# Kernel tuning notes

Hardware: AMD Instinct MI355X
Metric: run time of the kernel (lower is better)

Reference implementation:

```python
import jax, jax.numpy as jnp
import numpy as np

XS, YS = 512, 512  # xsize+1, ysize+1 with init args 511, 511


def _grid_sample_align_corners(img, gx, gy):
    """Bilinear grid_sample with align_corners=True, zeros padding.
    img: [C, H, W]; gx, gy: [X, Y] normalized coords in grid_sample convention
    (gx indexes W, gy indexes H). Returns [C, X, Y]."""
    C, H, W = img.shape
    x = (gx + 1.0) * 0.5 * (W - 1)
    y = (gy + 1.0) * 0.5 * (H - 1)
    x0 = jnp.floor(x)
    y0 = jnp.floor(y)
    wx1 = x - x0
    wy1 = y - y0
    out = jnp.zeros((C,) + gx.shape, img.dtype)
    for dy in (0, 1):
        for dx in (0, 1):
            xi = x0 + dx
            yi = y0 + dy
            w = (wx1 if dx else 1.0 - wx1) * (wy1 if dy else 1.0 - wy1)
            valid = (xi >= 0) & (xi <= W - 1) & (yi >= 0) & (yi <= H - 1)
            xc = jnp.clip(xi, 0, W - 1).astype(jnp.int32)
            yc = jnp.clip(yi, 0, H - 1).astype(jnp.int32)
            v = img[:, yc, xc]  # [C, X, Y]
            out = out + v * (w * valid.astype(img.dtype))[None]
    return out


def _per_batch(a, b, c, pnts, coors, contain):
    # a/b/c: [C,H,W] feature maps; pnts: [P,2] in [0,1]; coors: [P,3] int; contain: [P] int
    keep = contain > 0
    # route invalid pillars to an out-of-bounds index -> dropped by scatter
    cx = jnp.where(keep, coors[:, 1], XS)
    cy = jnp.where(keep, coors[:, 2], YS)
    grid = jnp.full((XS, YS, 2), -2.0, a.dtype)
    grid = grid.at[cx, cy, :].set(pnts * 2.0 - 1.0, mode='drop')
    mask = jnp.zeros((XS, YS), a.dtype).at[cx, cy].set(1.0, mode='drop')
    gx, gy = grid[..., 0], grid[..., 1]
    fa = _grid_sample_align_corners(a, gx, gy) * mask[None]
    fb = _grid_sample_align_corners(b, gx, gy) * mask[None]
    fc = _grid_sample_align_corners(c, gx, gy) * mask[None]
    return fa, fb, fc


def reference(c3, c4, c5, dynamic_img, pillar_img_pts, rgb_coors, contains_rgb):
    fa, fb, fc = jax.vmap(_per_batch)(c3, c4, c5, pillar_img_pts, rgb_coors, contains_rgb)
    # weighted fusion of the three scales, weights broadcast over channel dim
    return (fa * dynamic_img[:, 0:1]
            + fb * dynamic_img[:, 1:2]
            + fc * dynamic_img[:, 2:3])


def setup_inputs() -> dict:
    key = jax.random.key(0)
    ks = jax.random.split(key, 7)
    B, C, P = 4, 64, 20000
    c3 = jax.random.normal(ks[0], (B, C, 48, 160), jnp.float32)
    c4 = jax.random.normal(ks[1], (B, C, 24, 80), jnp.float32)
    c5 = jax.random.normal(ks[2], (B, C, 12, 40), jnp.float32)
    dynamic_img = jax.random.uniform(ks[3], (B, 3, XS, YS), jnp.float32)
    pillar_img_pts = jax.random.uniform(ks[4], (B, P, 2), jnp.float32)
    rgb_coors = jax.random.randint(ks[5], (B, P, 3), 0, 512, jnp.int32)
    contains_rgb = jax.random.randint(ks[6], (B, P), 0, 2, jnp.int32)
    return {"c3": c3, "c4": c4, "c5": c5, "dynamic_img": dynamic_img,
            "pillar_img_pts": pillar_img_pts, "rgb_coors": rgb_coors,
            "contains_rgb": contains_rgb}
```

## Files before the change

### kernel.cpp

```cpp
#include <hip/hip_runtime.h>
#include <cstddef>

#define XSZ 512
#define YSZ 512
#define NB  4
#define NC  64
#define NP  20000
#define H3 48
#define W3 160
#define H4 24
#define W4 80
#define H5 12
#define W5 40
#define HW3 (H3*W3)
#define HW4 (H4*W4)
#define HW5 (H5*W5)
#define SLOT_CAP 64

#define FILL_BLOCKS 256
#define T3_TILES (NB * ((HW3 + 63) / 64))
#define T4_TILES (NB * ((HW4 + 63) / 64))
#define T5_TILES (NB * ((HW5 + 63) / 64))

typedef float f4 __attribute__((ext_vector_type(4)));

__global__ void __launch_bounds__(256)
k_init(int4* __restrict__ winner4,
       const float* __restrict__ c3, const float* __restrict__ c4,
       const float* __restrict__ c5,
       float* __restrict__ c3t, float* __restrict__ c4t, float* __restrict__ c5t) {
    int blk = blockIdx.x;
    if (blk < FILL_BLOCKS) {
        int base = blk * 1024 + threadIdx.x;
        int4 m1 = make_int4(-1, -1, -1, -1);
        winner4[base      ] = m1;
        winner4[base + 256] = m1;
        winner4[base + 512] = m1;
        winner4[base + 768] = m1;
        return;
    }
    __shared__ float lds[NC * 65];
    int t = blk - FILL_BLOCKS;
    const float* in; float* outp; int HW, tpb;
    if (t < T3_TILES)                      { in = c3; outp = c3t; HW = HW3; tpb = 120; }
    else if ((t -= T3_TILES) < T4_TILES)   { in = c4; outp = c4t; HW = HW4; tpb = 30; }
    else { t -= T4_TILES;                    in = c5; outp = c5t; HW = HW5; tpb = 8; }
    int b  = t / tpb;
    int p0 = (t - b * tpb) * 64;
    int lane = threadIdx.x & 63, wave = threadIdx.x >> 6;
    const float* in_b  = in   + (size_t)b * NC * HW;
    float*       out_b = outp + (size_t)b * HW * NC;

    int p = p0 + lane;
    if (p < HW) {
        for (int ch = wave; ch < NC; ch += 4)
            lds[ch * 65 + lane] = in_b[(size_t)ch * HW + p];
    }
    __syncthreads();
    for (int pp = wave; pp < 64; pp += 4) {
        int pq = p0 + pp;
        if (pq < HW) out_b[(size_t)pq * NC + lane] = lds[lane * 65 + pp];
    }
}

__global__ void __launch_bounds__(256)
k_scatter(const int* __restrict__ coors, const int* __restrict__ contains,
          int* __restrict__ winner) {
    int idx = blockIdx.x * blockDim.x + threadIdx.x;
    if (idx >= NB * NP) return;
    if (contains[idx] <= 0) return;
    int b  = idx / NP;
    int p  = idx - b * NP;
    int cx = coors[idx * 3 + 1];
    int cy = coors[idx * 3 + 2];
    if ((unsigned)cx >= XSZ || (unsigned)cy >= YSZ) return;
    atomicMax(&winner[((size_t)b * XSZ + cx) * YSZ + cy], p);
}

__device__ __forceinline__ float bilinT(const float* __restrict__ img, int H, int W,
                                        float px, float py, int c) {
    float gx = px * 2.0f - 1.0f;
    float gy = py * 2.0f - 1.0f;
    float x = (gx + 1.0f) * 0.5f * (float)(W - 1);
    float y = (gy + 1.0f) * 0.5f * (float)(H - 1);
    float x0f = floorf(x), y0f = floorf(y);
    float wx1 = x - x0f,   wy1 = y - y0f;
    float wx0 = 1.0f - wx1, wy0 = 1.0f - wy1;
    int x0 = (int)x0f, y0 = (int)y0f;
    float acc = 0.0f;
#pragma unroll
    for (int dy = 0; dy < 2; ++dy) {
#pragma unroll
        for (int dx = 0; dx < 2; ++dx) {
            int xi = x0 + dx, yi = y0 + dy;
            bool valid = (xi >= 0) && (xi <= W - 1) && (yi >= 0) && (yi <= H - 1);
            int xc = min(max(xi, 0), W - 1);
            int yc = min(max(yi, 0), H - 1);
            float w = (dx ? wx1 : wx0) * (dy ? wy1 : wy0);
            float v = img[(size_t)(yc * W + xc) * NC + c];
            acc = fmaf(v, valid ? w : 0.0f, acc);
        }
    }
    return acc;
}

__device__ __forceinline__ float bilinG(const float* __restrict__ img, int H, int W,
                                        float px, float py, int c, int sChan) {
    float gx = px * 2.0f - 1.0f;
    float gy = py * 2.0f - 1.0f;
    float x = (gx + 1.0f) * 0.5f * (float)(W - 1);
    float y = (gy + 1.0f) * 0.5f * (float)(H - 1);
    float x0f = floorf(x), y0f = floorf(y);
    float wx1 = x - x0f,   wy1 = y - y0f;
    float wx0 = 1.0f - wx1, wy0 = 1.0f - wy1;
    int x0 = (int)x0f, y0 = (int)y0f;
    float acc = 0.0f;
#pragma unroll
    for (int dy = 0; dy < 2; ++dy) {
#pragma unroll
        for (int dx = 0; dx < 2; ++dx) {
            int xi = x0 + dx, yi = y0 + dy;
            bool valid = (xi >= 0) && (xi <= W - 1) && (yi >= 0) && (yi <= H - 1);
            int xc = min(max(xi, 0), W - 1);
            int yc = min(max(yi, 0), H - 1);
            float w = (dx ? wx1 : wx0) * (dy ? wy1 : wy0);
            float v = img[(size_t)(yc * W + xc) + (size_t)c * sChan];
            acc = fmaf(v, valid ? w : 0.0f, acc);
        }
    }
    return acc;
}

__global__ void __launch_bounds__(256)
k_fused(const float* __restrict__ pnts, const int* __restrict__ winner,
        const float* __restrict__ i3t, const float* __restrict__ i4t,
        const float* __restrict__ i5t, const float* __restrict__ dyn,
        float* __restrict__ out) {
    __shared__ float vec[SLOT_CAP * 65];
    __shared__ unsigned short smap[YSZ];
    __shared__ unsigned short slist[YSZ];
    __shared__ unsigned short ylist[YSZ];
    __shared__ int cnt;

    int bx = blockIdx.x;
    int b = bx >> 9, x = bx & 511;
    int tid = threadIdx.x;
    if (tid == 0) cnt = 0;
    __syncthreads();

    const int2* wrow2 = (const int2*)(winner + ((size_t)b * XSZ + x) * YSZ);
    int2 r2 = wrow2[tid];
    {
        int y0 = tid * 2;
        int pv0 = r2.x, pv1 = r2.y;
        int s0 = 0xFFFF, s1 = 0xFFFF;
        if (pv0 >= 0) { s0 = atomicAdd(&cnt, 1); slist[s0] = (unsigned short)pv0;
                        ylist[s0] = (unsigned short)y0; }
        if (pv1 >= 0) { s1 = atomicAdd(&cnt, 1); slist[s1] = (unsigned short)pv1;
                        ylist[s1] = (unsigned short)(y0 + 1); }
        smap[y0]     = (unsigned short)s0;
        smap[y0 + 1] = (unsigned short)s1;
    }
    __syncthreads();
    int n = cnt;
    int nB = min(n, SLOT_CAP);

    int wave = tid >> 6, lane = tid & 63;
    const float* i3b = i3t + (size_t)b * HW3 * NC;
    const float* i4b = i4t + (size_t)b * HW4 * NC;
    const float* i5b = i5t + (size_t)b * HW5 * NC;
    for (int s = wave; s < nB; s += 4) {
        int p = slist[s], y = ylist[s];
        int idx = b * NP + p;
        float px = pnts[idx * 2], py = pnts[idx * 2 + 1];
        float fa = bilinT(i3b, H3, W3, px, py, lane);
        float fb = bilinT(i4b, H4, W4, px, py, lane);
        float fc = bilinT(i5b, H5, W5, px, py, lane);
        size_t dbase = (((size_t)b * 3) * XSZ + x) * YSZ + y;
        float d0 = dyn[dbase];
        float d1 = dyn[dbase + (size_t)XSZ * YSZ];
        float d2 = dyn[dbase + (size_t)2 * XSZ * YSZ];
        vec[s * 65 + lane] = fa * d0 + fb * d1 + fc * d2;
    }
    __syncthreads();

    int lane_c = tid >> 7;
    int t7 = tid & 127;
    int y4 = t7 << 2;
    int s0 = smap[y4], s1 = smap[y4 + 1], s2 = smap[y4 + 2], s3 = smap[y4 + 3];
    bool h0 = s0 < SLOT_CAP, h1 = s1 < SLOT_CAP;
    bool h2 = s2 < SLOT_CAP, h3 = s3 < SLOT_CAP;
    size_t obase = (size_t)b * NC * XSZ * YSZ + (size_t)x * YSZ + y4;
    for (int cb = 0; cb < NC; cb += 2) {
        int c = cb + lane_c;
        f4 v = (f4)(0.0f);
        if (h0) v.x = vec[s0 * 65 + c];
        if (h1) v.y = vec[s1 * 65 + c];
        if (h2) v.z = vec[s2 * 65 + c];
        if (h3) v.w = vec[s3 * 65 + c];
        *(f4*)(out + obase + (size_t)c * (XSZ * YSZ)) = v;
    }

    if (n > SLOT_CAP) {
        __syncthreads();
        for (int s = SLOT_CAP + wave; s < n; s += 4) {
            int p = slist[s], y = ylist[s];
            int idx = b * NP + p;
            float px = pnts[idx * 2], py = pnts[idx * 2 + 1];
            float fa = bilinT(i3b, H3, W3, px, py, lane);
            float fb = bilinT(i4b, H4, W4, px, py, lane);
            float fc = bilinT(i5b, H5, W5, px, py, lane);
            size_t dbase = (((size_t)b * 3) * XSZ + x) * YSZ + y;
            float d0 = dyn[dbase];
            float d1 = dyn[dbase + (size_t)XSZ * YSZ];
            float d2 = dyn[dbase + (size_t)2 * XSZ * YSZ];
            out[(((size_t)b * NC + lane) * XSZ + x) * YSZ + y] =
                fa * d0 + fb * d1 + fc * d2;
        }
    }
}

__global__ void __launch_bounds__(256)
k_samp_fb(const int* __restrict__ coors, const int* __restrict__ contains,
          const float* __restrict__ pnts, const int* __restrict__ winner,
          const float* __restrict__ i3, const float* __restrict__ i4,
          const float* __restrict__ i5, const float* __restrict__ dyn,
          float* __restrict__ out) {
    int nw   = gridDim.x << 2;
    int wv   = (blockIdx.x << 2) + (threadIdx.x >> 6);
    int lane = threadIdx.x & 63;
    for (int idx = wv; idx < NB * NP; idx += nw) {
        if (contains[idx] <= 0) continue;
        int b = idx / NP;
        int p = idx - b * NP;
        int cx = coors[idx * 3 + 1];
        int cy = coors[idx * 3 + 2];
        if ((unsigned)cx >= XSZ || (unsigned)cy >= YSZ) continue;
        if (winner[((size_t)b * XSZ + cx) * YSZ + cy] != p) continue;
        float px = pnts[idx * 2], py = pnts[idx * 2 + 1];
        float fa = bilinG(i3 + (size_t)b * NC * HW3, H3, W3, px, py, lane, HW3);
        float fb = bilinG(i4 + (size_t)b * NC * HW4, H4, W4, px, py, lane, HW4);
        float fc = bilinG(i5 + (size_t)b * NC * HW5, H5, W5, px, py, lane, HW5);
        size_t dbase = (((size_t)b * 3) * XSZ + cx) * YSZ + cy;
        float d0 = dyn[dbase];
        float d1 = dyn[dbase + (size_t)XSZ * YSZ];
        float d2 = dyn[dbase + (size_t)2 * XSZ * YSZ];
        out[(((size_t)b * NC + lane) * XSZ + cx) * YSZ + cy] = fa * d0 + fb * d1 + fc * d2;
    }
}

__global__ void k_zero4(float4* __restrict__ p, long n4) {
    long i = (long)blockIdx.x * blockDim.x + threadIdx.x;
    long stride = (long)gridDim.x * blockDim.x;
    for (; i < n4; i += stride) p[i] = make_float4(0.f, 0.f, 0.f, 0.f);
}

extern "C" void kernel_launch(void* const* d_in, const int* in_sizes, int n_in,
                              void* d_out, int out_size, void* d_ws, size_t ws_size,
                              hipStream_t stream) {
    const float* c3       = (const float*)d_in[0];
    const float* c4       = (const float*)d_in[1];
    const float* c5       = (const float*)d_in[2];
    const float* dyn      = (const float*)d_in[3];
    const float* pnts     = (const float*)d_in[4];
    const int*   coors    = (const int*)d_in[5];
    const int*   contains = (const int*)d_in[6];
    float* out = (float*)d_out;

    char* ws = (char*)d_ws;
    size_t off = 0;
    int* winner = (int*)(ws + off);   off += (size_t)NB * XSZ * YSZ * 4;
    float* c3t  = (float*)(ws + off); off += (size_t)NB * NC * HW3 * 4;
    float* c4t  = (float*)(ws + off); off += (size_t)NB * NC * HW4 * 4;
    float* c5t  = (float*)(ws + off); off += (size_t)NB * NC * HW5 * 4;
    size_t t_need = off;
    bool useT = (ws_size >= t_need);

    int npts = NB * NP;
    int init_blocks = useT ? (FILL_BLOCKS + T3_TILES + T4_TILES + T5_TILES)
                           : FILL_BLOCKS;
    k_init<<<init_blocks, 256, 0, stream>>>((int4*)winner, c3, c4, c5,
                                            c3t, c4t, c5t);
    k_scatter<<<(npts + 255) / 256, 256, 0, stream>>>(coors, contains, winner);

    if (useT) {
        k_fused<<<NB * XSZ, 256, 0, stream>>>(pnts, winner, c3t, c4t, c5t,
                                              dyn, out);
    } else {
        long n4 = (long)out_size / 4;
        k_zero4<<<8192, 256, 0, stream>>>((float4*)out, n4);
        k_samp_fb<<<2048, 256, 0, stream>>>(coors, contains, pnts, winner,
                                            c3, c4, c5, dyn, out);
    }
}
```

Baseline: 78.55 us.

## Merge init, scatter and gather into one cooperative persistent kernel

Replaces the three separate launches (winner fill plus transpose, scatter, fused gather) with one cooperative kernel of 1024 blocks. Grid-wide syncs separate the phases, and each block then handles two x-rows with 4 pixels per thread and a larger slot cap. The goal is to remove launch gaps and kernel-boundary drains. In exchange it relies on cooperative launch co-residency, adds the cost of grid syncs, and falls back to a memset-based path if the launch fails.

```diff
diff --git a/kernel.cpp b/kernel.cpp
--- a/kernel.cpp
+++ b/kernel.cpp
@@ -1,4 +1,5 @@
 #include <hip/hip_runtime.h>
+#include <hip/hip_cooperative_groups.h>
 #include <cstddef>
 
 #define XSZ 512
@@ -15,51 +16,205 @@
 #define HW3 (H3*W3)
 #define HW4 (H4*W4)
 #define HW5 (H5*W5)
-#define SLOT_CAP 64
-
-#define FILL_BLOCKS 256
+#define HWO (XSZ*YSZ)
+
+#define GRID2 1024
+#define CAP   96
+
 #define T3_TILES (NB * ((HW3 + 63) / 64))
 #define T4_TILES (NB * ((HW4 + 63) / 64))
 #define T5_TILES (NB * ((HW5 + 63) / 64))
+#define T_TOTAL  (T3_TILES + T4_TILES + T5_TILES)
+#define SCAT_BLOCKS ((NB * NP + 255) / 256)
 
 typedef float f4 __attribute__((ext_vector_type(4)));
 
-__global__ void __launch_bounds__(256)
-k_init(int4* __restrict__ winner4,
-       const float* __restrict__ c3, const float* __restrict__ c4,
-       const float* __restrict__ c5,
-       float* __restrict__ c3t, float* __restrict__ c4t, float* __restrict__ c5t) {
-    int blk = blockIdx.x;
-    if (blk < FILL_BLOCKS) {
-        int base = blk * 1024 + threadIdx.x;
-        int4 m1 = make_int4(-1, -1, -1, -1);
-        winner4[base      ] = m1;
-        winner4[base + 256] = m1;
-        winner4[base + 512] = m1;
-        winner4[base + 768] = m1;
-        return;
-    }
-    __shared__ float lds[NC * 65];
-    int t = blk - FILL_BLOCKS;
-    const float* in; float* outp; int HW, tpb;
-    if (t < T3_TILES)                      { in = c3; outp = c3t; HW = HW3; tpb = 120; }
-    else if ((t -= T3_TILES) < T4_TILES)   { in = c4; outp = c4t; HW = HW4; tpb = 30; }
-    else { t -= T4_TILES;                    in = c5; outp = c5t; HW = HW5; tpb = 8; }
-    int b  = t / tpb;
-    int p0 = (t - b * tpb) * 64;
-    int lane = threadIdx.x & 63, wave = threadIdx.x >> 6;
-    const float* in_b  = in   + (size_t)b * NC * HW;
-    float*       out_b = outp + (size_t)b * HW * NC;
-
-    int p = p0 + lane;
-    if (p < HW) {
-        for (int ch = wave; ch < NC; ch += 4)
-            lds[ch * 65 + lane] = in_b[(size_t)ch * HW + p];
-    }
+__device__ __forceinline__ float bilinT(const float* __restrict__ img, int H, int W,
+                                        float px, float py, int c) {
+    float gx = px * 2.0f - 1.0f;
+    float gy = py * 2.0f - 1.0f;
+    float x = (gx + 1.0f) * 0.5f * (float)(W - 1);
+    float y = (gy + 1.0f) * 0.5f * (float)(H - 1);
+    float x0f = floorf(x), y0f = floorf(y);
+    float wx1 = x - x0f,   wy1 = y - y0f;
+    float wx0 = 1.0f - wx1, wy0 = 1.0f - wy1;
+    int x0 = (int)x0f, y0 = (int)y0f;
+    float acc = 0.0f;
+#pragma unroll
+    for (int dy = 0; dy < 2; ++dy) {
+#pragma unroll
+        for (int dx = 0; dx < 2; ++dx) {
+            int xi = x0 + dx, yi = y0 + dy;
+            bool valid = (xi >= 0) && (xi <= W - 1) && (yi >= 0) && (yi <= H - 1);
+            int xc = min(max(xi, 0), W - 1);
+            int yc = min(max(yi, 0), H - 1);
+            float w = (dx ? wx1 : wx0) * (dy ? wy1 : wy0);
+            float v = img[(size_t)(yc * W + xc) * NC + c];
+            acc = fmaf(v, valid ? w : 0.0f, acc);
+        }
+    }
+    return acc;
+}
+
+__device__ __forceinline__ float bilinG(const float* __restrict__ img, int H, int W,
+                                        float px, float py, int c, int sChan) {
+    float gx = px * 2.0f - 1.0f;
+    float gy = py * 2.0f - 1.0f;
+    float x = (gx + 1.0f) * 0.5f * (float)(W - 1);
+    float y = (gy + 1.0f) * 0.5f * (float)(H - 1);
+    float x0f = floorf(x), y0f = floorf(y);
+    float wx1 = x - x0f,   wy1 = y - y0f;
+    float wx0 = 1.0f - wx1, wy0 = 1.0f - wy1;
+    int x0 = (int)x0f, y0 = (int)y0f;
+    float acc = 0.0f;
+#pragma unroll
+    for (int dy = 0; dy < 2; ++dy) {
+#pragma unroll
+        for (int dx = 0; dx < 2; ++dx) {
+            int xi = x0 + dx, yi = y0 + dy;
+            bool valid = (xi >= 0) && (xi <= W - 1) && (yi >= 0) && (yi <= H - 1);
+            int xc = min(max(xi, 0), W - 1);
+            int yc = min(max(yi, 0), H - 1);
+            float w = (dx ? wx1 : wx0) * (dy ? wy1 : wy0);
+            float v = img[(size_t)(yc * W + xc) + (size_t)c * sChan];
+            acc = fmaf(v, valid ? w : 0.0f, acc);
+        }
+    }
+    return acc;
+}
+
+__global__ void __launch_bounds__(256, 4)
+k_all(const float* __restrict__ c3, const float* __restrict__ c4,
+      const float* __restrict__ c5,
+      float* __restrict__ c3t, float* __restrict__ c4t, float* __restrict__ c5t,
+      const float* __restrict__ dyn, const float* __restrict__ pnts,
+      const int* __restrict__ coors, const int* __restrict__ contains,
+      int* __restrict__ winner, float* __restrict__ out) {
+    __shared__ float vec[CAP * 65];
+    __shared__ unsigned short smap[1024];
+    __shared__ unsigned int   slist[1024];
+    __shared__ int cnt;
+
+    cooperative_groups::grid_group grid = cooperative_groups::this_grid();
+    int bx  = blockIdx.x;
+    int tid = threadIdx.x;
+
+    ((int4*)winner)[bx * 256 + tid] = make_int4(-1, -1, -1, -1);
+    grid.sync();
+
+    if (bx < T_TOTAL) {
+        float* tl = vec;
+        int t = bx;
+        const float* in; float* outp; int HW, tpb;
+        if (t < T3_TILES)                    { in = c3; outp = c3t; HW = HW3; tpb = 120; }
+        else if ((t -= T3_TILES) < T4_TILES) { in = c4; outp = c4t; HW = HW4; tpb = 30; }
+        else { t -= T4_TILES;                  in = c5; outp = c5t; HW = HW5; tpb = 8; }
+        int b  = t / tpb;
+        int p0 = (t - b * tpb) * 64;
+        int lane = tid & 63, wave = tid >> 6;
+        const float* in_b  = in   + (size_t)b * NC * HW;
+        float*       out_b = outp + (size_t)b * HW * NC;
+        int p = p0 + lane;
+        if (p < HW) {
+            for (int ch = wave; ch < NC; ch += 4)
+                tl[ch * 65 + lane] = in_b[(size_t)ch * HW + p];
+        }
+        __syncthreads();
+        for (int pp = wave; pp < 64; pp += 4) {
+            int pq = p0 + pp;
+            if (pq < HW) out_b[(size_t)pq * NC + lane] = tl[lane * 65 + pp];
+        }
+    } else if (bx < T_TOTAL + SCAT_BLOCKS) {
+        int idx = (bx - T_TOTAL) * 256 + tid;
+        if (idx < NB * NP && contains[idx] > 0) {
+            int b  = idx / NP;
+            int p  = idx - b * NP;
+            int cx = coors[idx * 3 + 1];
+            int cy = coors[idx * 3 + 2];
+            if ((unsigned)cx < XSZ && (unsigned)cy < YSZ)
+                atomicMax(&winner[((size_t)b * XSZ + cx) * YSZ + cy], p);
+        }
+    }
+    grid.sync();
+
+    int b  = bx >> 8;
+    int x0 = (bx & 255) << 1;
+
+    if (tid == 0) cnt = 0;
     __syncthreads();
-    for (int pp = wave; pp < 64; pp += 4) {
-        int pq = p0 + pp;
-        if (pq < HW) out_b[(size_t)pq * NC + lane] = lds[lane * 65 + pp];
+
+    const int4* wr = (const int4*)(winner + ((size_t)b * XSZ + x0) * YSZ);
+    int4 r = wr[tid];
+    {
+        int f0 = tid * 4;
+        int pv[4] = { r.x, r.y, r.z, r.w };
+#pragma unroll
+        for (int j = 0; j < 4; ++j) {
+            unsigned short s = 0xFFFF;
+            if (pv[j] >= 0) {
+                int sl = atomicAdd(&cnt, 1);
+                slist[sl] = ((unsigned)pv[j] << 10) | (unsigned)(f0 + j);
+                s = (unsigned short)sl;
+            }
+            smap[f0 + j] = s;
+        }
+    }
+    __syncthreads();
+    int n  = cnt;
+    int nB = min(n, CAP);
+
+    int wave = tid >> 6, lane = tid & 63;
+    const float* i3b = c3t + (size_t)b * HW3 * NC;
+    const float* i4b = c4t + (size_t)b * HW4 * NC;
+    const float* i5b = c5t + (size_t)b * HW5 * NC;
+    for (int s = wave; s < nB; s += 4) {
+        unsigned pk = slist[s];
+        int p = pk >> 10, f = pk & 1023;
+        int xs = x0 + (f >> 9), y = f & 511;
+        int idx = b * NP + p;
+        float px = pnts[idx * 2], py = pnts[idx * 2 + 1];
+        float fa = bilinT(i3b, H3, W3, px, py, lane);
+        float fb = bilinT(i4b, H4, W4, px, py, lane);
+        float fc = bilinT(i5b, H5, W5, px, py, lane);
+        size_t dbase = (((size_t)b * 3) * XSZ + xs) * YSZ + y;
+        float d0 = dyn[dbase];
+        float d1 = dyn[dbase + (size_t)XSZ * YSZ];
+        float d2 = dyn[dbase + (size_t)2 * XSZ * YSZ];
+        vec[s * 65 + lane] = fa * d0 + fb * d1 + fc * d2;
+    }
+    __syncthreads();
+
+    int f0 = tid * 4;
+    int s0 = smap[f0], s1 = smap[f0 + 1], s2 = smap[f0 + 2], s3 = smap[f0 + 3];
+    bool h0 = s0 < CAP, h1 = s1 < CAP, h2 = s2 < CAP, h3 = s3 < CAP;
+    size_t obase = (size_t)b * NC * HWO + (size_t)x0 * YSZ + f0;
+    for (int c = 0; c < NC; ++c) {
+        f4 v = (f4)(0.0f);
+        if (h0) v.x = vec[s0 * 65 + c];
+        if (h1) v.y = vec[s1 * 65 + c];
+        if (h2) v.z = vec[s2 * 65 + c];
+        if (h3) v.w = vec[s3 * 65 + c];
+        *(f4*)(out + obase + (size_t)c * HWO) = v;
+    }
+
+    if (n > CAP) {
+        __syncthreads();
+        for (int s = CAP + wave; s < n; s += 4) {
+            unsigned pk = slist[s];
+            int p = pk >> 10, f = pk & 1023;
+            int xs = x0 + (f >> 9), y = f & 511;
+            int idx = b * NP + p;
+            float px = pnts[idx * 2], py = pnts[idx * 2 + 1];
+            float fa = bilinT(i3b, H3, W3, px, py, lane);
+            float fb = bilinT(i4b, H4, W4, px, py, lane);
+            float fc = bilinT(i5b, H5, W5, px, py, lane);
+            size_t dbase = (((size_t)b * 3) * XSZ + xs) * YSZ + y;
+            float d0 = dyn[dbase];
+            float d1 = dyn[dbase + (size_t)XSZ * YSZ];
+            float d2 = dyn[dbase + (size_t)2 * XSZ * YSZ];
+            out[(((size_t)b * NC + lane) * XSZ + xs) * YSZ + y] =
+                fa * d0 + fb * d1 + fc * d2;
+        }
     }
 }
 
@@ -75,149 +230,6 @@
     int cy = coors[idx * 3 + 2];
     if ((unsigned)cx >= XSZ || (unsigned)cy >= YSZ) return;
     atomicMax(&winner[((size_t)b * XSZ + cx) * YSZ + cy], p);
-}
-
-__device__ __forceinline__ float bilinT(const float* __restrict__ img, int H, int W,
-                                        float px, float py, int c) {
-    float gx = px * 2.0f - 1.0f;
-    float gy = py * 2.0f - 1.0f;
-    float x = (gx + 1.0f) * 0.5f * (float)(W - 1);
-    float y = (gy + 1.0f) * 0.5f * (float)(H - 1);
-    float x0f = floorf(x), y0f = floorf(y);
-    float wx1 = x - x0f,   wy1 = y - y0f;
-    float wx0 = 1.0f - wx1, wy0 = 1.0f - wy1;
-    int x0 = (int)x0f, y0 = (int)y0f;
-    float acc = 0.0f;
-#pragma unroll
-    for (int dy = 0; dy < 2; ++dy) {
-#pragma unroll
-        for (int dx = 0; dx < 2; ++dx) {
-            int xi = x0 + dx, yi = y0 + dy;
-            bool valid = (xi >= 0) && (xi <= W - 1) && (yi >= 0) && (yi <= H - 1);
-            int xc = min(max(xi, 0), W - 1);
-            int yc = min(max(yi, 0), H - 1);
-            float w = (dx ? wx1 : wx0) * (dy ? wy1 : wy0);
-            float v = img[(size_t)(yc * W + xc) * NC + c];
-            acc = fmaf(v, valid ? w : 0.0f, acc);
-        }
-    }
-    return acc;
-}
-
-__device__ __forceinline__ float bilinG(const float* __restrict__ img, int H, int W,
-                                        float px, float py, int c, int sChan) {
-    float gx = px * 2.0f - 1.0f;
-    float gy = py * 2.0f - 1.0f;
-    float x = (gx + 1.0f) * 0.5f * (float)(W - 1);
-    float y = (gy + 1.0f) * 0.5f * (float)(H - 1);
-    float x0f = floorf(x), y0f = floorf(y);
-    float wx1 = x - x0f,   wy1 = y - y0f;
-    float wx0 = 1.0f - wx1, wy0 = 1.0f - wy1;
-    int x0 = (int)x0f, y0 = (int)y0f;
-    float acc = 0.0f;
-#pragma unroll
-    for (int dy = 0; dy < 2; ++dy) {
-#pragma unroll
-        for (int dx = 0; dx < 2; ++dx) {
-            int xi = x0 + dx, yi = y0 + dy;
-            bool valid = (xi >= 0) && (xi <= W - 1) && (yi >= 0) && (yi <= H - 1);
-            int xc = min(max(xi, 0), W - 1);
-            int yc = min(max(yi, 0), H - 1);
-            float w = (dx ? wx1 : wx0) * (dy ? wy1 : wy0);
-            float v = img[(size_t)(yc * W + xc) + (size_t)c * sChan];
-            acc = fmaf(v, valid ? w : 0.0f, acc);
-        }
-    }
-    return acc;
-}
-
-__global__ void __launch_bounds__(256)
-k_fused(const float* __restrict__ pnts, const int* __restrict__ winner,
-        const float* __restrict__ i3t, const float* __restrict__ i4t,
-        const float* __restrict__ i5t, const float* __restrict__ dyn,
-        float* __restrict__ out) {
-    __shared__ float vec[SLOT_CAP * 65];
-    __shared__ unsigned short smap[YSZ];
-    __shared__ unsigned short slist[YSZ];
-    __shared__ unsigned short ylist[YSZ];
-    __shared__ int cnt;
-
-    int bx = blockIdx.x;
-    int b = bx >> 9, x = bx & 511;
-    int tid = threadIdx.x;
-    if (tid == 0) cnt = 0;
-    __syncthreads();
-
-    const int2* wrow2 = (const int2*)(winner + ((size_t)b * XSZ + x) * YSZ);
-    int2 r2 = wrow2[tid];
-    {
-        int y0 = tid * 2;
-        int pv0 = r2.x, pv1 = r2.y;
-        int s0 = 0xFFFF, s1 = 0xFFFF;
-        if (pv0 >= 0) { s0 = atomicAdd(&cnt, 1); slist[s0] = (unsigned short)pv0;
-                        ylist[s0] = (unsigned short)y0; }
-        if (pv1 >= 0) { s1 = atomicAdd(&cnt, 1); slist[s1] = (unsigned short)pv1;
-                        ylist[s1] = (unsigned short)(y0 + 1); }
-        smap[y0]     = (unsigned short)s0;
-        smap[y0 + 1] = (unsigned short)s1;
-    }
-    __syncthreads();
-    int n = cnt;
-    int nB = min(n, SLOT_CAP);
-
-    int wave = tid >> 6, lane = tid & 63;
-    const float* i3b = i3t + (size_t)b * HW3 * NC;
-    const float* i4b = i4t + (size_t)b * HW4 * NC;
-    const float* i5b = i5t + (size_t)b * HW5 * NC;
-    for (int s = wave; s < nB; s += 4) {
-        int p = slist[s], y = ylist[s];
-        int idx = b * NP + p;
-        float px = pnts[idx * 2], py = pnts[idx * 2 + 1];
-        float fa = bilinT(i3b, H3, W3, px, py, lane);
-        float fb = bilinT(i4b, H4, W4, px, py, lane);
-        float fc = bilinT(i5b, H5, W5, px, py, lane);
-        size_t dbase = (((size_t)b * 3) * XSZ + x) * YSZ + y;
-        float d0 = dyn[dbase];
-        float d1 = dyn[dbase + (size_t)XSZ * YSZ];
-        float d2 = dyn[dbase + (size_t)2 * XSZ * YSZ];
-        vec[s * 65 + lane] = fa * d0 + fb * d1 + fc * d2;
-    }
-    __syncthreads();
-
-    int lane_c = tid >> 7;
-    int t7 = tid & 127;
-    int y4 = t7 << 2;
-    int s0 = smap[y4], s1 = smap[y4 + 1], s2 = smap[y4 + 2], s3 = smap[y4 + 3];
-    bool h0 = s0 < SLOT_CAP, h1 = s1 < SLOT_CAP;
-    bool h2 = s2 < SLOT_CAP, h3 = s3 < SLOT_CAP;
-    size_t obase = (size_t)b * NC * XSZ * YSZ + (size_t)x * YSZ + y4;
-    for (int cb = 0; cb < NC; cb += 2) {
-        int c = cb + lane_c;
-        f4 v = (f4)(0.0f);
-        if (h0) v.x = vec[s0 * 65 + c];
-        if (h1) v.y = vec[s1 * 65 + c];
-        if (h2) v.z = vec[s2 * 65 + c];
-        if (h3) v.w = vec[s3 * 65 + c];
-        *(f4*)(out + obase + (size_t)c * (XSZ * YSZ)) = v;
-    }
-
-    if (n > SLOT_CAP) {
-        __syncthreads();
-        for (int s = SLOT_CAP + wave; s < n; s += 4) {
-            int p = slist[s], y = ylist[s];
-            int idx = b * NP + p;
-            float px = pnts[idx * 2], py = pnts[idx * 2 + 1];
-            float fa = bilinT(i3b, H3, W3, px, py, lane);
-            float fb = bilinT(i4b, H4, W4, px, py, lane);
-            float fc = bilinT(i5b, H5, W5, px, py, lane);
-            size_t dbase = (((size_t)b * 3) * XSZ + x) * YSZ + y;
-            float d0 = dyn[dbase];
-            float d1 = dyn[dbase + (size_t)XSZ * YSZ];
-            float d2 = dyn[dbase + (size_t)2 * XSZ * YSZ];
-            out[(((size_t)b * NC + lane) * XSZ + x) * YSZ + y] =
-                fa * d0 + fb * d1 + fc * d2;
-        }
-    }
 }
 
 __global__ void __launch_bounds__(256)
@@ -276,17 +288,23 @@
     size_t t_need = off;
     bool useT = (ws_size >= t_need);
 
-    int npts = NB * NP;
-    int init_blocks = useT ? (FILL_BLOCKS + T3_TILES + T4_TILES + T5_TILES)
-                           : FILL_BLOCKS;
-    k_init<<<init_blocks, 256, 0, stream>>>((int4*)winner, c3, c4, c5,
-                                            c3t, c4t, c5t);
-    k_scatter<<<(npts + 255) / 256, 256, 0, stream>>>(coors, contains, winner);
-
+    bool launched = false;
     if (useT) {
-        k_fused<<<NB * XSZ, 256, 0, stream>>>(pnts, winner, c3t, c4t, c5t,
-                                              dyn, out);
-    } else {
+        void* args[12] = {
+            (void*)&c3, (void*)&c4, (void*)&c5,
+            (void*)&c3t, (void*)&c4t, (void*)&c5t,
+            (void*)&dyn, (void*)&pnts, (void*)&coors, (void*)&contains,
+            (void*)&winner, (void*)&out
+        };
+        hipError_t e = hipLaunchCooperativeKernel((void*)k_all, dim3(GRID2),
+                                                  dim3(256), args, 0, stream);
+        launched = (e == hipSuccess);
+    }
+
+    if (!launched) {
+        int npts = NB * NP;
+        hipMemsetAsync(winner, 0xFF, (size_t)NB * XSZ * YSZ * 4, stream);
+        k_scatter<<<(npts + 255) / 256, 256, 0, stream>>>(coors, contains, winner);
         long n4 = (long)out_size / 4;
         k_zero4<<<8192, 256, 0, stream>>>((float4*)out, n4);
         k_samp_fb<<<2048, 256, 0, stream>>>(coors, contains, pnts, winner,
```

Measured after the change: 248.2 us. 216% more time.
